# Optimization experiments

Measured on AMD Instinct MI355X. Metric: run time of the kernel, lower is better.

The kernel has to match this reference:

```python
import jax, jax.numpy as jnp
import numpy as np

H = 128
R = 14
B = 2048
TYPES = ['operator', 'table', 'column', 'predicate', 'operation', 'literal', 'numeral']
SIZES = {'operator': 100000, 'table': 20000, 'column': 120000, 'predicate': 60000,
         'operation': 100000, 'literal': 50000, 'numeral': 50000}
FEAT = {'operator': 4, 'table': 2, 'column': 10, 'predicate': 4, 'operation': 8,
        'literal': 1, 'numeral': 1}
# (name, src_type, dst_type, num_edges), order matches edge_type_mapping in the torch module
EDGES = [('ei_scannedby', 'table', 'operator', 100000),
         ('ei_pred_filters', 'predicate', 'operator', 100000),
         ('ei_outputby', 'column', 'operator', 100000),
         ('ei_col_connects', 'column', 'operation', 100000),
         ('ei_calledby', 'operator', 'operator', 100000),
         ('ei_op_filters', 'operation', 'operator', 100000),
         ('ei_op_connects', 'operation', 'predicate', 100000),
         ('ei_lit_connects', 'literal', 'operation', 100000),
         ('ei_num_connects', 'numeral', 'operation', 100000),
         ('ei_lit_self', 'literal', 'literal', 50000),
         ('ei_num_self', 'numeral', 'numeral', 50000),
         ('ei_tab_self', 'table', 'table', 20000),
         ('ei_col_self', 'column', 'column', 120000),
         ('ei_pred_self', 'predicate', 'predicate', 60000)]
OFFS = {}
_o = 0
for _t in TYPES:
    OFFS[_t] = _o
    _o += SIZES[_t]
N_TOTAL = _o


def setup_inputs():
    key = jax.random.key(0)
    ks = iter(jax.random.split(key, 64))
    inp = {}
    for t in TYPES:
        inp['x_' + t] = jax.random.normal(next(ks), (SIZES[t], FEAT[t]), jnp.float32)
    for name, s, d, E in EDGES:
        src = jax.random.randint(next(ks), (E,), 0, SIZES[s], jnp.int32)
        dst = jax.random.randint(next(ks), (E,), 0, SIZES[d], jnp.int32)
        inp[name] = jnp.stack([src, dst])
    inp['batch_operator'] = jnp.sort(
        jax.random.randint(next(ks), (SIZES['operator'],), 0, B, jnp.int32))

    def lin_w(k, din, dout):
        s = 1.0 / float(np.sqrt(din))
        return jax.random.uniform(k, (din, dout), jnp.float32, -s, s)

    for t in TYPES:
        inp['W_' + t] = lin_w(next(ks), FEAT[t], H)
        inp['b_' + t] = jnp.zeros((H,), jnp.float32)
    for c in ('c1', 'c2'):
        inp[c + '_root'] = lin_w(next(ks), H, H)
        inp[c + '_rel'] = jax.random.normal(next(ks), (R, H, H), jnp.float32) / float(np.sqrt(H))
        inp[c + '_bias'] = jnp.zeros((H,), jnp.float32)
    inp['n1_g'] = jnp.ones((H,), jnp.float32); inp['n1_b'] = jnp.zeros((H,), jnp.float32)
    inp['n2_g'] = jnp.ones((H,), jnp.float32); inp['n2_b'] = jnp.zeros((H,), jnp.float32)
    inp['W_lin'] = lin_w(next(ks), H, 1)
    inp['b_lin'] = jnp.zeros((1,), jnp.float32)
    return inp


def layer_norm(x, g, b, eps=1e-5):
    mu = jnp.mean(x, axis=-1, keepdims=True)
    var = jnp.var(x, axis=-1, keepdims=True)
    return (x - mu) * jax.lax.rsqrt(var + eps) * g + b


def rgcn(x, rel_edges, w_root, w_rel, bias):
    # PyG RGCNConv: root transform + per-relation gather -> GEMM -> scatter-mean into dst
    out = x @ w_root
    for r, (src, dst) in enumerate(rel_edges):
        msg = x[src] @ w_rel[r]  # [E_r, H]
        agg = jax.ops.segment_sum(msg, dst, num_segments=N_TOTAL)
        cnt = jax.ops.segment_sum(jnp.ones(src.shape, x.dtype), dst, num_segments=N_TOTAL)
        out = out + agg / jnp.maximum(cnt, 1.0)[:, None]
    return out + bias


def reference(x_operator, x_table, x_column, x_predicate, x_operation, x_literal, x_numeral,
              ei_scannedby, ei_pred_filters, ei_outputby, ei_col_connects, ei_calledby,
              ei_op_filters, ei_op_connects, ei_lit_connects, ei_num_connects, ei_lit_self,
              ei_num_self, ei_tab_self, ei_col_self, ei_pred_self, batch_operator,
              W_operator, b_operator, W_table, b_table, W_column, b_column,
              W_predicate, b_predicate, W_operation, b_operation, W_literal, b_literal,
              W_numeral, b_numeral, c1_root, c1_rel, c1_bias, c2_root, c2_rel, c2_bias,
              n1_g, n1_b, n2_g, n2_b, W_lin, b_lin):
    # per-node-type input embedding, then concat in fixed type order
    x = jnp.concatenate([
        x_operator @ W_operator + b_operator,
        x_table @ W_table + b_table,
        x_column @ W_column + b_column,
        x_predicate @ W_predicate + b_predicate,
        x_operation @ W_operation + b_operation,
        x_literal @ W_literal + b_literal,
        x_numeral @ W_numeral + b_numeral], axis=0)
    eis = [ei_scannedby, ei_pred_filters, ei_outputby, ei_col_connects, ei_calledby,
           ei_op_filters, ei_op_connects, ei_lit_connects, ei_num_connects, ei_lit_self,
           ei_num_self, ei_tab_self, ei_col_self, ei_pred_self]
    rel_edges = [(e[0] + OFFS[s], e[1] + OFFS[d]) for e, (_, s, d, _) in zip(eis, EDGES)]
    h = rgcn(x, rel_edges, c1_root, c1_rel, c1_bias)
    h = layer_norm(jax.nn.elu(h), n1_g, n1_b)  # dropout is identity in eval mode
    h = rgcn(h, rel_edges, c2_root, c2_rel, c2_bias)
    h = layer_norm(jax.nn.elu(h), n2_g, n2_b)
    op = h[:SIZES['operator']]  # operator offset is 0
    cnt = jax.ops.segment_sum(jnp.ones((op.shape[0],), op.dtype), batch_operator, num_segments=B)
    pooled = jax.ops.segment_sum(op, batch_operator, num_segments=B) / jnp.maximum(cnt, 1.0)[:, None]
    return (pooled @ W_lin + b_lin)[:, 0]  # [B]
```

## Files before the change

### kernel.cpp

```cpp
#include <hip/hip_runtime.h>
#include <hip/hip_bf16.h>
#include <math.h>

#define HD 128
#define N_OP 100000
#define N_L1 400000
#define NB 2048
#define CNT_TOT 1160000
#define EDG_TOT 1100000

typedef short short8 __attribute__((ext_vector_type(8)));
typedef float floatx4 __attribute__((ext_vector_type(4)));

static const int REL_E[14]    = {100000,100000,100000,100000,100000,100000,100000,100000,100000,50000,50000,20000,120000,60000};
static const int REL_DSZ[14]  = {100000,100000,100000,100000,100000,100000,60000,100000,100000,50000,50000,20000,120000,60000};
static const int CNT_OFF[14]  = {0,100000,200000,300000,400000,500000,600000,660000,760000,860000,910000,960000,980000,1100000};
static const int SRC_T[14] = {1,3,2,2,0,4,4,5,6,5,6,1,2,3};
static const int TF[7]  = {4,2,10,4,8,1,1};
static const size_t AGR_OFF[14] = {0,200000,600000,1600000,2600000,3000000,3800000,4280000,4380000,0,0,4480000,4520000,5720000};
#define AGR_TOT 5960000
static const int RELW[14] = {4,7,12,93,23,28,70,104,106,-1,-1,40,54,79};
static const int RELI[14] = {6,11,22,103,27,36,78,105,107,-1,-1,42,64,83};
static const int ROOTW[5] = {0,38,44,66,85};
static const int ROOTB[5] = {37,43,65,84,108};
#define WL1_ROWS 109

__device__ inline unsigned short f2bf(float f) {
  union { float f; unsigned int u; } v; v.f = f;
  unsigned int r = v.u + 0x7FFF + ((v.u >> 16) & 1);
  return (unsigned short)(r >> 16);
}
__device__ inline float bfu2f(unsigned short u) {
  union { unsigned int i; float f; } v; v.i = ((unsigned int)u) << 16; return v.f;
}

struct CJob { const int* dst; int coff; int E; int blk0; };
struct CPackK { CJob j[12]; int bblk0; const int* batch; float* pcnt; int nop; };

__global__ void count_k(CPackK P, int* __restrict__ ICNT) {
  int b = blockIdx.x;
  if (b >= P.bblk0) {
    int i = (b - P.bblk0) * 256 + threadIdx.x;
    if (i < P.nop) atomicAdd(&P.pcnt[P.batch[i]], 1.0f);
    return;
  }
  int ji = 0;
#pragma unroll
  for (int i = 1; i < 12; ++i) if (b >= P.j[i].blk0) ji = i;
  CJob J = P.j[ji];
  int e = (b - J.blk0) * 256 + threadIdx.x;
  if (e < J.E) atomicAdd(&ICNT[J.coff + J.dst[e]], 1);
}

#define SCAN_BLK 1024
__global__ void scan1(const int* __restrict__ in, int* __restrict__ out,
                      int* __restrict__ bsum, int n) {
  __shared__ int sh[256];
  int t = threadIdx.x;
  int base = blockIdx.x * SCAN_BLK + t * 4;
  int v0 = 0, v1 = 0, v2 = 0, v3 = 0;
  if (base + 3 < n) { int4 q = *(const int4*)&in[base]; v0 = q.x; v1 = q.y; v2 = q.z; v3 = q.w; }
  else {
    if (base < n) v0 = in[base];
    if (base + 1 < n) v1 = in[base + 1];
    if (base + 2 < n) v2 = in[base + 2];
    if (base + 3 < n) v3 = in[base + 3];
  }
  int ts = v0 + v1 + v2 + v3;
  sh[t] = ts; __syncthreads();
  for (int o = 1; o < 256; o <<= 1) {
    int x = (t >= o) ? sh[t - o] : 0;
    __syncthreads();
    sh[t] += x;
    __syncthreads();
  }
  int excl = sh[t] - ts;
  if (base < n) out[base] = excl;
  if (base + 1 < n) out[base + 1] = excl + v0;
  if (base + 2 < n) out[base + 2] = excl + v0 + v1;
  if (base + 3 < n) out[base + 3] = excl + v0 + v1 + v2;
  if (t == 255) bsum[blockIdx.x] = sh[255];
}

__global__ void scan2(int* __restrict__ bs, int nb) {
  __shared__ int sh[256];
  int t = threadIdx.x;
  const int C = 5;
  int v[C]; int ts = 0;
#pragma unroll
  for (int i = 0; i < C; ++i) { int idx = t * C + i; v[i] = (idx < nb) ? bs[idx] : 0; ts += v[i]; }
  sh[t] = ts; __syncthreads();
  for (int o = 1; o < 256; o <<= 1) {
    int x = (t >= o) ? sh[t - o] : 0;
    __syncthreads();
    sh[t] += x;
    __syncthreads();
  }
  int run = sh[t] - ts;
#pragma unroll
  for (int i = 0; i < C; ++i) { int idx = t * C + i; if (idx < nb) bs[idx] = run; run += v[i]; }
}

__global__ void scan3(int* __restrict__ CUR, int2* __restrict__ OFF2,
                      const int* __restrict__ ICNT, const int* __restrict__ bs, int n) {
  int i = blockIdx.x * 256 + threadIdx.x;
  if (i < n) {
    int o = CUR[i] + bs[i >> 10];
    CUR[i] = o;
    OFF2[i] = make_int2(o, ICNT[i]);
  }
}

struct FJob { const int* src; const int* dst; int coff; int E; int blk0; };
struct FPackK { FJob j[12]; };

__global__ void fill_k(FPackK P, int* __restrict__ CUR, int* __restrict__ EDG) {
  int b = blockIdx.x;
  int ji = 0;
#pragma unroll
  for (int i = 1; i < 12; ++i) if (b >= P.j[i].blk0) ji = i;
  FJob J = P.j[ji];
  int e = (b - J.blk0) * 256 + threadIdx.x;
  if (e < J.E) {
    int pos = atomicAdd(&CUR[J.coff + J.dst[e]], 1);
    EDG[pos] = J.src[e];
  }
}

struct GJob { const float* x; float* agr; int coff; int D; int F; int blk0; };
struct GPack { GJob j[12]; };

template <int F>
__device__ inline void gathF(const float* __restrict__ x, float* __restrict__ agr,
                             const int* __restrict__ EDG, int2 oc, int d) {
  if (oc.y == 0) return;
  float s[F];
#pragma unroll
  for (int f = 0; f < F; ++f) s[f] = 0.f;
  for (int e = 0; e < oc.y; ++e) {
    int si = EDG[oc.x + e];
    const float* xp = &x[(size_t)si * F];
#pragma unroll
    for (int f = 0; f < F; ++f) s[f] += xp[f];
  }
  float rc = 1.0f / (float)oc.y;
  float* ap = &agr[(size_t)d * F];
#pragma unroll
  for (int f = 0; f < F; ++f) ap[f] = s[f] * rc;
}

__global__ void gather_all(GPack P, const int2* __restrict__ OFF2, const int* __restrict__ EDG) {
  int b = blockIdx.x;
  int ji = 0;
#pragma unroll
  for (int i = 1; i < 12; ++i) if (b >= P.j[i].blk0) ji = i;
  GJob J = P.j[ji];
  int d = (b - J.blk0) * 256 + threadIdx.x;
  if (d >= J.D) return;
  int2 oc = OFF2[J.coff + d];
  switch (J.F) {
    case 1:  gathF<1>(J.x, J.agr, EDG, oc, d); break;
    case 2:  gathF<2>(J.x, J.agr, EDG, oc, d); break;
    case 4:  gathF<4>(J.x, J.agr, EDG, oc, d); break;
    case 8:  gathF<8>(J.x, J.agr, EDG, oc, d); break;
    default: gathF<10>(J.x, J.agr, EDG, oc, d); break;
  }
}

struct CombJob { const float* A; const float* bin; const float* Mtx; const float* extra; float* Wout; float* bout; int F; };
struct CombPack { CombJob j[17]; };

__global__ void weights_prep(CombPack P, const float* __restrict__ c2root,
                             const float* __restrict__ c2rel, __hip_bfloat16* __restrict__ Wt) {
  int b = blockIdx.x;
  if (b < 17) {
    if (threadIdx.x >= 128) return;
    CombJob J = P.j[b];
    int c = threadIdx.x;
    for (int f = 0; f <= J.F; ++f) {
      const float* arow = (f < J.F) ? &J.A[f * HD] : J.bin;
      float s = (f < J.F) ? 0.f : (J.extra ? J.extra[c] : 0.f);
      for (int k = 0; k < HD; ++k) s = fmaf(arow[k], J.Mtx[k * HD + c], s);
      if (f < J.F) J.Wout[f * HD + c] = s;
      else J.bout[c] = s;
    }
  } else {
    const int RID[6] = {-1, 0, 1, 2, 4, 5};
    int j = b - 17;
    const float* W = (j == 0) ? c2root : (c2rel + (size_t)RID[j] * HD * HD);
    __hip_bfloat16* o = Wt + (size_t)j * HD * 136;
    for (int i = threadIdx.x; i < HD * HD; i += 256) {
      int k = i >> 7, n = i & 127;
      o[n * 136 + k] = __float2bfloat16(W[i]);
    }
  }
}

struct L1v2 {
  const float* x0; const float* x1; const float* x2; const float* x3; const float* x4;
  const float* AGR; const float* WL1; const int2* OFF2;
  const float* g; const float* b;
  unsigned short* Hb;
};

__device__ inline void ldv2(float* s, const float* __restrict__ p) {
  float2 v = *(const float2*)p; s[0] = v.x; s[1] = v.y;
}
__device__ inline void ldv4(float* s, const float* __restrict__ p) {
  float4 v = *(const float4*)p; s[0] = v.x; s[1] = v.y; s[2] = v.z; s[3] = v.w;
}
__device__ inline void relF1(float* s, const float* __restrict__ agr,
                             const int2* __restrict__ OFF2, int cb, int row) {
  if (OFF2[cb + row].y > 0) { s[0] = agr[row]; s[1] = 1.f; }
  else { s[0] = 0.f; s[1] = 0.f; }
}
__device__ inline void relF2(float* s, const float* __restrict__ agr,
                             const int2* __restrict__ OFF2, int cb, int row) {
  if (OFF2[cb + row].y > 0) { ldv2(s, &agr[(size_t)row * 2]); s[2] = 1.f; }
  else { s[0] = s[1] = s[2] = 0.f; }
}
__device__ inline void relF4(float* s, const float* __restrict__ agr,
                             const int2* __restrict__ OFF2, int cb, int row) {
  if (OFF2[cb + row].y > 0) { ldv4(s, &agr[(size_t)row * 4]); s[4] = 1.f; }
  else {
#pragma unroll
    for (int f = 0; f < 5; ++f) s[f] = 0.f;
  }
}
__device__ inline void relF8(float* s, const float* __restrict__ agr,
                             const int2* __restrict__ OFF2, int cb, int row) {
  if (OFF2[cb + row].y > 0) {
    ldv4(s, &agr[(size_t)row * 8]); ldv4(s + 4, &agr[(size_t)row * 8 + 4]); s[8] = 1.f;
  } else {
#pragma unroll
    for (int f = 0; f < 9; ++f) s[f] = 0.f;
  }
}
__device__ inline void relF10(float* s, const float* __restrict__ agr,
                              const int2* __restrict__ OFF2, int cb, int row) {
  if (OFF2[cb + row].y > 0) {
    const float* p = &agr[(size_t)row * 10];
#pragma unroll
    for (int j = 0; j < 5; ++j) ldv2(s + 2 * j, p + 2 * j);
    s[10] = 1.f;
  } else {
#pragma unroll
    for (int f = 0; f < 11; ++f) s[f] = 0.f;
  }
}

template <int KT>
__device__ inline void l1_dot8(const float* __restrict__ Ls, const float (&s)[KT],
                               int c4, float (&a)[8]) {
  {
    float4 w0 = *(const float4*)&Ls[KT * 128 + c4];
    float4 w1 = *(const float4*)&Ls[KT * 128 + c4 + 64];
    a[0] = w0.x; a[1] = w0.y; a[2] = w0.z; a[3] = w0.w;
    a[4] = w1.x; a[5] = w1.y; a[6] = w1.z; a[7] = w1.w;
  }
#pragma unroll
  for (int k = 0; k < KT; ++k) {
    float4 w0 = *(const float4*)&Ls[k * 128 + c4];
    float4 w1 = *(const float4*)&Ls[k * 128 + c4 + 64];
    a[0] = fmaf(s[k], w0.x, a[0]); a[1] = fmaf(s[k], w0.y, a[1]);
    a[2] = fmaf(s[k], w0.z, a[2]); a[3] = fmaf(s[k], w0.w, a[3]);
    a[4] = fmaf(s[k], w1.x, a[4]); a[5] = fmaf(s[k], w1.y, a[5]);
    a[6] = fmaf(s[k], w1.z, a[6]); a[7] = fmaf(s[k], w1.w, a[7]);
  }
}

__device__ inline void l1_fin8(float (&a)[8], int c4, const float* __restrict__ g,
                               const float* __restrict__ bb,
                               unsigned short* __restrict__ Hb, int orow) {
  float p = 0.f, q = 0.f;
#pragma unroll
  for (int j = 0; j < 8; ++j) {
    a[j] = (a[j] > 0.f) ? a[j] : (expf(a[j]) - 1.f);
    p += a[j]; q += a[j] * a[j];
  }
#pragma unroll
  for (int m = 8; m >= 1; m >>= 1) {
    p += __shfl_xor(p, m, 64);
    q += __shfl_xor(q, m, 64);
  }
  float mean = p * (1.0f / HD);
  float var = q * (1.0f / HD) - mean * mean;
  float rstd = rsqrtf(var + 1e-5f);
  float4 g0 = *(const float4*)&g[c4], g1 = *(const float4*)&g[c4 + 64];
  float4 b0 = *(const float4*)&bb[c4], b1 = *(const float4*)&bb[c4 + 64];
  float gg[8] = {g0.x, g0.y, g0.z, g0.w, g1.x, g1.y, g1.z, g1.w};
  float bv[8] = {b0.x, b0.y, b0.z, b0.w, b1.x, b1.y, b1.z, b1.w};
  float o[8];
#pragma unroll
  for (int j = 0; j < 8; ++j) o[j] = (a[j] - mean) * rstd * gg[j] + bv[j];
  uint2 lo, hi;
  lo.x = (unsigned int)f2bf(o[0]) | ((unsigned int)f2bf(o[1]) << 16);
  lo.y = (unsigned int)f2bf(o[2]) | ((unsigned int)f2bf(o[3]) << 16);
  hi.x = (unsigned int)f2bf(o[4]) | ((unsigned int)f2bf(o[5]) << 16);
  hi.y = (unsigned int)f2bf(o[6]) | ((unsigned int)f2bf(o[7]) << 16);
  *(uint2*)&Hb[(size_t)orow * HD + c4] = lo;
  *(uint2*)&Hb[(size_t)orow * HD + c4 + 64] = hi;
}

__global__ __launch_bounds__(256) void layer1_v5(L1v2 A) {
  __shared__ float Ls[38 * 128];
  const int b = blockIdx.x, t = threadIdx.x;
  const int wv = t >> 6, ln = t & 63;
  const int sub = ln >> 4, c4 = (ln & 15) * 4;
  int type, seg;
  if (b < 1563) { type = 0; seg = b; }
  else if (b < 1876) { type = 1; seg = b - 1563; }
  else if (b < 3751) { type = 2; seg = b - 1876; }
  else if (b < 4689) { type = 3; seg = b - 3751; }
  else { type = 4; seg = b - 4689; }
  const int NR[5] = {38, 6, 22, 19, 24};
  const int RB[5] = {0, 38, 44, 66, 85};
  const int TR[5] = {100000, 20000, 120000, 60000, 100000};
  const int OB[5] = {0, 100000, 120000, 240000, 300000};
  {
    const float4* src = (const float4*)(A.WL1 + RB[type] * 128);
    float4* dst = (float4*)Ls;
    int n4 = NR[type] * 32;
    for (int i = t; i < n4; i += 256) dst[i] = src[i];
  }
  __syncthreads();
  const int row0 = seg * 64, M = TR[type], ob = OB[type];

  if (type == 0) {
#pragma unroll
    for (int it = 0; it < 4; ++it) {
      int row = row0 + it * 16 + wv * 4 + sub;
      if (row >= M) continue;
      float s[37];
      ldv4(s, &A.x0[(size_t)row * 4]);
      relF2(s + 4, A.AGR + 0, A.OFF2, 0, row);
      relF4(s + 7, A.AGR + 200000, A.OFF2, 100000, row);
      relF10(s + 12, A.AGR + 600000, A.OFF2, 200000, row);
      relF4(s + 23, A.AGR + 2600000, A.OFF2, 400000, row);
      relF8(s + 28, A.AGR + 3000000, A.OFF2, 500000, row);
      float a[8];
      l1_dot8<37>(Ls, s, c4, a);
      l1_fin8(a, c4, A.g, A.b, A.Hb, ob + row);
    }
  } else if (type == 1) {
#pragma unroll
    for (int it = 0; it < 4; ++it) {
      int row = row0 + it * 16 + wv * 4 + sub;
      if (row >= M) continue;
      float s[5];
      ldv2(s, &A.x1[(size_t)row * 2]);
      relF2(s + 2, A.AGR + 4480000, A.OFF2, 960000, row);
      float a[8];
      l1_dot8<5>(Ls, s, c4, a);
      l1_fin8(a, c4, A.g, A.b, A.Hb, ob + row);
    }
  } else if (type == 2) {
#pragma unroll
    for (int it = 0; it < 4; ++it) {
      int row = row0 + it * 16 + wv * 4 + sub;
      if (row >= M) continue;
      float s[21];
      const float* p = &A.x2[(size_t)row * 10];
#pragma unroll
      for (int j = 0; j < 5; ++j) ldv2(s + 2 * j, p + 2 * j);
      relF10(s + 10, A.AGR + 4520000, A.OFF2, 980000, row);
      float a[8];
      l1_dot8<21>(Ls, s, c4, a);
      l1_fin8(a, c4, A.g, A.b, A.Hb, ob + row);
    }
  } else if (type == 3) {
#pragma unroll
    for (int it = 0; it < 4; ++it) {
      int row = row0 + it * 16 + wv * 4 + sub;
      if (row >= M) continue;
      float s[18];
      ldv4(s, &A.x3[(size_t)row * 4]);
      relF8(s + 4, A.AGR + 3800000, A.OFF2, 600000, row);
      relF4(s + 13, A.AGR + 5720000, A.OFF2, 1100000, row);
      float a[8];
      l1_dot8<18>(Ls, s, c4, a);
      l1_fin8(a, c4, A.g, A.b, A.Hb, ob + row);
    }
  } else {
#pragma unroll
    for (int it = 0; it < 4; ++it) {
      int row = row0 + it * 16 + wv * 4 + sub;
      if (row >= M) continue;
      float s[23];
      ldv4(s, &A.x4[(size_t)row * 8]);
      ldv4(s + 4, &A.x4[(size_t)row * 8 + 4]);
      relF10(s + 8, A.AGR + 1600000, A.OFF2, 300000, row);
      relF1(s + 19, A.AGR + 4280000, A.OFF2, 660000, row);
      relF1(s + 21, A.AGR + 4380000, A.OFF2, 760000, row);
      float a[8];
      l1_dot8<23>(Ls, s, c4, a);
      l1_fin8(a, c4, A.g, A.b, A.Hb, ob + row);
    }
  }
}

__global__ __launch_bounds__(256, 3)
void l2_fused(const unsigned short* __restrict__ Hb, const unsigned short* __restrict__ Wall,
              const int2* __restrict__ OFF2, const int* __restrict__ EDG,
              const float* __restrict__ c2bias, const float* __restrict__ n2g,
              const float* __restrict__ n2b, const float* __restrict__ Wl,
              const int* __restrict__ batch, float* __restrict__ accb, int M) {
  const int CSR_OFF[5] = {0, 100000, 200000, 400000, 500000};
  const int SOFF[5]    = {100000, 240000, 120000, 0, 300000};
  __shared__ unsigned short Ws[128 * 136];
  const int t = threadIdx.x, wv = t >> 6, ln = t & 63;
  const int quad = ln >> 4, ln15 = ln & 15, q8 = quad * 8;
  const int m0 = blockIdx.x * 128;

  int2 ocs[2][5];
#pragma unroll
  for (int mt = 0; mt < 2; ++mt) {
    int rowA = m0 + (wv * 2 + mt) * 16 + ln15;
#pragma unroll
    for (int r = 0; r < 5; ++r)
      ocs[mt][r] = (rowA < M) ? OFF2[CSR_OFF[r] + rowA] : make_int2(0, 0);
  }

  float bias_c[8], gw[8];
  float pg = 0.f, pb = 0.f;
#pragma unroll
  for (int nt = 0; nt < 8; ++nt) {
    int col = nt * 16 + ln15;
    float wl = Wl[col], gc = n2g[col], bc = n2b[col];
    bias_c[nt] = c2bias[col];
    gw[nt] = gc * wl;
    pg += gc * wl;
    pb += bc * wl;
  }
#pragma unroll
  for (int m = 8; m >= 1; m >>= 1) {
    pg += __shfl_xor(pg, m, 64);
    pb += __shfl_xor(pb, m, 64);
  }

  floatx4 acc[2][8];
#pragma unroll
  for (int a = 0; a < 2; ++a)
#pragma unroll
    for (int b = 0; b < 8; ++b) acc[a][b] = (floatx4){0.f, 0.f, 0.f, 0.f};

  for (int term = 0; term < 6; ++term) {
    __syncthreads();
    {
      const uint4* wg = (const uint4*)(Wall + (size_t)term * 128 * 136);
      uint4* ws4 = (uint4*)Ws;
#pragma unroll
      for (int i = 0; i < 9; ++i) {
        int idx = i * 256 + t;
        if (idx < 2176) ws4[idx] = wg[idx];
      }
    }
    __syncthreads();

    short8 afr[2][4];
#pragma unroll
    for (int mt = 0; mt < 2; ++mt) {
      int rowA = m0 + (wv * 2 + mt) * 16 + ln15;
      if (term == 0) {
        if (rowA < M) {
#pragma unroll
          for (int k4 = 0; k4 < 4; ++k4)
            afr[mt][k4] = *(const short8*)&Hb[(size_t)rowA * HD + k4 * 32 + q8];
        } else {
#pragma unroll
          for (int k4 = 0; k4 < 4; ++k4)
#pragma unroll
            for (int j = 0; j < 8; ++j) afr[mt][k4][j] = 0;
        }
      } else {
        float sum[4][8];
#pragma unroll
        for (int k4 = 0; k4 < 4; ++k4)
#pragma unroll
          for (int j = 0; j < 8; ++j) sum[k4][j] = 0.f;
        int2 oc = ocs[mt][term - 1];
        if (oc.y > 0) {
          int so = SOFF[term - 1];
          for (int e = 0; e < oc.y; ++e) {
            size_t s = (size_t)(EDG[oc.x + e] + so);
#pragma unroll
            for (int k4 = 0; k4 < 4; ++k4) {
              short8 h = *(const short8*)&Hb[s * HD + k4 * 32 + q8];
#pragma unroll
              for (int j = 0; j < 8; ++j) sum[k4][j] += bfu2f((unsigned short)h[j]);
            }
          }
          float rc = 1.0f / (float)oc.y;
#pragma unroll
          for (int k4 = 0; k4 < 4; ++k4)
#pragma unroll
            for (int j = 0; j < 8; ++j) sum[k4][j] *= rc;
        }
#pragma unroll
        for (int k4 = 0; k4 < 4; ++k4)
#pragma unroll
          for (int j = 0; j < 8; ++j) afr[mt][k4][j] = (short)f2bf(sum[k4][j]);
      }
    }

#pragma unroll
    for (int nt = 0; nt < 8; ++nt) {
      int wrow = nt * 16 + ln15;
      short8 b0 = *(const short8*)&Ws[wrow * 136 + 0 + q8];
      short8 b1 = *(const short8*)&Ws[wrow * 136 + 32 + q8];
      short8 b2 = *(const short8*)&Ws[wrow * 136 + 64 + q8];
      short8 b3 = *(const short8*)&Ws[wrow * 136 + 96 + q8];
#pragma unroll
      for (int mt = 0; mt < 2; ++mt) {
        acc[mt][nt] = __builtin_amdgcn_mfma_f32_16x16x32_bf16(afr[mt][0], b0, acc[mt][nt], 0, 0, 0);
        acc[mt][nt] = __builtin_amdgcn_mfma_f32_16x16x32_bf16(afr[mt][1], b1, acc[mt][nt], 0, 0, 0);
        acc[mt][nt] = __builtin_amdgcn_mfma_f32_16x16x32_bf16(afr[mt][2], b2, acc[mt][nt], 0, 0, 0);
        acc[mt][nt] = __builtin_amdgcn_mfma_f32_16x16x32_bf16(afr[mt][3], b3, acc[mt][nt], 0, 0, 0);
      }
    }
  }

#pragma unroll
  for (int mt = 0; mt < 2; ++mt) {
#pragma unroll
    for (int r = 0; r < 4; ++r) {
      int rowD = m0 + (wv * 2 + mt) * 16 + quad * 4 + r;
      float p = 0.f, q = 0.f, s1 = 0.f;
#pragma unroll
      for (int nt = 0; nt < 8; ++nt) {
        float v = acc[mt][nt][r] + bias_c[nt];
        float e = (v > 0.f) ? v : (expf(v) - 1.f);
        p += e; q += e * e; s1 += e * gw[nt];
      }
#pragma unroll
      for (int m = 8; m >= 1; m >>= 1) {
        p += __shfl_xor(p, m, 64);
        q += __shfl_xor(q, m, 64);
        s1 += __shfl_xor(s1, m, 64);
      }
      if (ln15 == 0 && rowD < M) {
        float mean = p * (1.0f / HD);
        float var = q * (1.0f / HD) - mean * mean;
        float rstd = rsqrtf(var + 1e-5f);
        float o = rstd * (s1 - mean * pg) + pb;
        atomicAdd(&accb[batch[rowD]], o);
      }
    }
  }
}

__global__ void final_kernel(const float* __restrict__ accb, const float* __restrict__ pcnt,
                             const float* __restrict__ bl, float* __restrict__ out) {
  int b = blockIdx.x * 256 + threadIdx.x;
  if (b < NB) out[b] = accb[b] / fmaxf(pcnt[b], 1.0f) + bl[0];
}

extern "C" void kernel_launch(void* const* d_in, const int* in_sizes, int n_in,
                              void* d_out, int out_size, void* d_ws, size_t ws_size,
                              hipStream_t stream) {
  const float* xt[7];
  for (int t = 0; t < 7; ++t) xt[t] = (const float*)d_in[t];
  const int* ei[14];
  for (int r = 0; r < 14; ++r) ei[r] = (const int*)d_in[7 + r];
  const int* batch = (const int*)d_in[21];
  const float* Wemb[7]; const float* bemb[7];
  for (int t = 0; t < 7; ++t) { Wemb[t] = (const float*)d_in[22 + 2 * t]; bemb[t] = (const float*)d_in[23 + 2 * t]; }
  const float* c_root[2] = {(const float*)d_in[36], (const float*)d_in[39]};
  const float* c_rel[2]  = {(const float*)d_in[37], (const float*)d_in[40]};
  const float* c_bias[2] = {(const float*)d_in[38], (const float*)d_in[41]};
  const float* ng[2] = {(const float*)d_in[42], (const float*)d_in[44]};
  const float* nbv[2] = {(const float*)d_in[43], (const float*)d_in[45]};
  const float* Wlin = (const float*)d_in[46];
  const float* blin = (const float*)d_in[47];
  float* out = (float*)d_out;

  char* base = (char*)d_ws;
  size_t off = 0;
  auto alloc = [&](size_t bytes) -> void* {
    void* p = base + off;
    off += (bytes + 255) & ~(size_t)255;
    return p;
  };
  __hip_bfloat16* Hb = (__hip_bfloat16*)alloc((size_t)N_L1 * HD * 2);
  float* AGR  = (float*)alloc((size_t)AGR_TOT * 4);
  int*   ICNT = (int*)alloc((size_t)CNT_TOT * 4);
  int*   CUR  = (int*)alloc((size_t)CNT_TOT * 4);
  int2*  OFF2 = (int2*)alloc((size_t)CNT_TOT * 8);
  int*   EDG  = (int*)alloc((size_t)EDG_TOT * 4);
  int*   BS   = (int*)alloc((size_t)1152 * 4);
  float* WL1  = (float*)alloc((size_t)WL1_ROWS * 128 * 4);
  __hip_bfloat16* WT2 = (__hip_bfloat16*)alloc((size_t)6 * HD * 136 * 2);
  float* ACC  = (float*)alloc((size_t)NB * 4);
  float* PCNT = (float*)alloc((size_t)NB * 4);

  static const int l1_rels[12] = {0,1,2,3,4,5,6,7,8,11,12,13};

  hipMemsetAsync(ICNT, 0, (size_t)CNT_TOT * 4, stream);
  hipMemsetAsync(ACC, 0, (size_t)2 * NB * 4, stream);

  CPackK CP1;
  int blk = 0;
  for (int q = 0; q < 12; ++q) {
    int r = l1_rels[q];
    CP1.j[q].dst = ei[r] + REL_E[r];
    CP1.j[q].coff = CNT_OFF[r];
    CP1.j[q].E = REL_E[r];
    CP1.j[q].blk0 = blk;
    blk += (REL_E[r] + 255) / 256;
  }
  CP1.bblk0 = blk; CP1.batch = batch; CP1.pcnt = PCNT; CP1.nop = N_OP;
  blk += (N_OP + 255) / 256;
  count_k<<<blk, 256, 0, stream>>>(CP1, ICNT);

  int nb1 = (CNT_TOT + SCAN_BLK - 1) / SCAN_BLK;
  scan1<<<nb1, 256, 0, stream>>>(ICNT, CUR, BS, CNT_TOT);
  scan2<<<1, 256, 0, stream>>>(BS, nb1);
  scan3<<<(CNT_TOT + 255) / 256, 256, 0, stream>>>(CUR, OFF2, ICNT, BS, CNT_TOT);

  FPackK FP;
  blk = 0;
  for (int q = 0; q < 12; ++q) {
    int r = l1_rels[q];
    FP.j[q].src = ei[r];
    FP.j[q].dst = ei[r] + REL_E[r];
    FP.j[q].coff = CNT_OFF[r];
    FP.j[q].E = REL_E[r];
    FP.j[q].blk0 = blk;
    blk += (REL_E[r] + 255) / 256;
  }
  fill_k<<<blk, 256, 0, stream>>>(FP, CUR, EDG);

  CombPack CP;
  for (int q = 0; q < 12; ++q) {
    int r = l1_rels[q]; int t = SRC_T[r];
    CombJob& J = CP.j[q];
    J.A = Wemb[t]; J.bin = bemb[t]; J.Mtx = c_rel[0] + (size_t)r * HD * HD;
    J.extra = nullptr;
    J.Wout = WL1 + (size_t)RELW[r] * 128;
    J.bout = WL1 + (size_t)RELI[r] * 128;
    J.F = TF[t];
  }
  for (int t = 0; t < 5; ++t) {
    CombJob& J = CP.j[12 + t];
    J.A = Wemb[t]; J.bin = bemb[t]; J.Mtx = c_root[0];
    J.extra = c_bias[0];
    J.Wout = WL1 + (size_t)ROOTW[t] * 128;
    J.bout = WL1 + (size_t)ROOTB[t] * 128;
    J.F = TF[t];
  }
  weights_prep<<<23, 256, 0, stream>>>(CP, c_root[1], c_rel[1], WT2);

  GPack GP;
  blk = 0;
  for (int q = 0; q < 12; ++q) {
    int r = l1_rels[q]; int t = SRC_T[r];
    GP.j[q].x = xt[t];
    GP.j[q].agr = AGR + AGR_OFF[r];
    GP.j[q].coff = CNT_OFF[r];
    GP.j[q].D = REL_DSZ[r];
    GP.j[q].F = TF[t];
    GP.j[q].blk0 = blk;
    blk += (REL_DSZ[r] + 255) / 256;
  }
  gather_all<<<blk, 256, 0, stream>>>(GP, OFF2, EDG);

  L1v2 A;
  A.x0 = xt[0]; A.x1 = xt[1]; A.x2 = xt[2]; A.x3 = xt[3]; A.x4 = xt[4];
  A.AGR = AGR; A.WL1 = WL1; A.OFF2 = OFF2;
  A.g = ng[0]; A.b = nbv[0]; A.Hb = (unsigned short*)Hb;
  layer1_v5<<<6252, 256, 0, stream>>>(A);

  l2_fused<<<(N_OP + 127) / 128, 256, 0, stream>>>(
      (const unsigned short*)Hb, (const unsigned short*)WT2,
      OFF2, EDG, c_bias[1], ng[1], nbv[1], Wlin, batch, ACC, N_OP);

  final_kernel<<<(NB + 255) / 256, 256, 0, stream>>>(ACC, PCNT, blin, out);
}
```

Measured before the change: 652.5 us.

## Pre-swizzle layer-2 weights into MFMA fragment order and drop LDS staging

Weights for the second layer are now written by the prep kernel directly in per-lane MFMA B-fragment order, so each wave reads its B fragments straight from global memory (L2-cached) instead of staging them through shared memory with two barriers per term. Each wave now handles one 16-row tile instead of two, the block covers 64 rows, and launch bounds allow 4 blocks per CU. The aim is to remove the barrier stalls and shared-memory footprint so more waves can hide the latency of the irregular neighbour gathers. The cost is repeated global weight reads per wave and half the reuse of each B fragment across row tiles.

Result: faster. 602.7 us (-7.6%).

```diff
diff --git a/kernel.cpp b/kernel.cpp
--- a/kernel.cpp
+++ b/kernel.cpp
@@ -188,10 +188,16 @@
     const int RID[6] = {-1, 0, 1, 2, 4, 5};
     int j = b - 17;
     const float* W = (j == 0) ? c2root : (c2rel + (size_t)RID[j] * HD * HD);
-    __hip_bfloat16* o = Wt + (size_t)j * HD * 136;
-    for (int i = threadIdx.x; i < HD * HD; i += 256) {
-      int k = i >> 7, n = i & 127;
-      o[n * 136 + k] = __float2bfloat16(W[i]);
+    __hip_bfloat16* o = Wt + (size_t)j * 16384;
+    for (int i = threadIdx.x; i < 16384; i += 256) {
+      int i8 = i & 7;
+      int ln = (i >> 3) & 63;
+      int k4 = (i >> 9) & 3;
+      int nt = i >> 11;
+      int ln15 = ln & 15, quad = ln >> 4;
+      int k = k4 * 32 + quad * 8 + i8;
+      int n = nt * 16 + ln15;
+      o[i] = __float2bfloat16(W[k * 128 + n]);
     }
   }
 }
@@ -399,27 +405,23 @@
   }
 }
 
-__global__ __launch_bounds__(256, 3)
-void l2_fused(const unsigned short* __restrict__ Hb, const unsigned short* __restrict__ Wall,
+__global__ __launch_bounds__(256, 4)
+void l2_fused(const unsigned short* __restrict__ Hb, const unsigned short* __restrict__ Wt,
               const int2* __restrict__ OFF2, const int* __restrict__ EDG,
               const float* __restrict__ c2bias, const float* __restrict__ n2g,
               const float* __restrict__ n2b, const float* __restrict__ Wl,
               const int* __restrict__ batch, float* __restrict__ accb, int M) {
   const int CSR_OFF[5] = {0, 100000, 200000, 400000, 500000};
   const int SOFF[5]    = {100000, 240000, 120000, 0, 300000};
-  __shared__ unsigned short Ws[128 * 136];
   const int t = threadIdx.x, wv = t >> 6, ln = t & 63;
   const int quad = ln >> 4, ln15 = ln & 15, q8 = quad * 8;
-  const int m0 = blockIdx.x * 128;
-
-  int2 ocs[2][5];
-#pragma unroll
-  for (int mt = 0; mt < 2; ++mt) {
-    int rowA = m0 + (wv * 2 + mt) * 16 + ln15;
-#pragma unroll
-    for (int r = 0; r < 5; ++r)
-      ocs[mt][r] = (rowA < M) ? OFF2[CSR_OFF[r] + rowA] : make_int2(0, 0);
-  }
+  const int m0 = blockIdx.x * 64;
+  const int rowA = m0 + wv * 16 + ln15;
+
+  int2 ocs[5];
+#pragma unroll
+  for (int r = 0; r < 5; ++r)
+    ocs[r] = (rowA < M) ? OFF2[CSR_OFF[r] + rowA] : make_int2(0, 0);
 
   float bias_c[8], gw[8];
   float pg = 0.f, pb = 0.f;
@@ -438,113 +440,89 @@
     pb += __shfl_xor(pb, m, 64);
   }
 
-  floatx4 acc[2][8];
-#pragma unroll
-  for (int a = 0; a < 2; ++a)
-#pragma unroll
-    for (int b = 0; b < 8; ++b) acc[a][b] = (floatx4){0.f, 0.f, 0.f, 0.f};
+  floatx4 acc[8];
+#pragma unroll
+  for (int b = 0; b < 8; ++b) acc[b] = (floatx4){0.f, 0.f, 0.f, 0.f};
 
   for (int term = 0; term < 6; ++term) {
-    __syncthreads();
-    {
-      const uint4* wg = (const uint4*)(Wall + (size_t)term * 128 * 136);
-      uint4* ws4 = (uint4*)Ws;
-#pragma unroll
-      for (int i = 0; i < 9; ++i) {
-        int idx = i * 256 + t;
-        if (idx < 2176) ws4[idx] = wg[idx];
+    short8 afr[4];
+    if (term == 0) {
+      if (rowA < M) {
+#pragma unroll
+        for (int k4 = 0; k4 < 4; ++k4)
+          afr[k4] = *(const short8*)&Hb[(size_t)rowA * HD + k4 * 32 + q8];
+      } else {
+#pragma unroll
+        for (int k4 = 0; k4 < 4; ++k4)
+#pragma unroll
+          for (int j = 0; j < 8; ++j) afr[k4][j] = 0;
       }
-    }
-    __syncthreads();
-
-    short8 afr[2][4];
-#pragma unroll
-    for (int mt = 0; mt < 2; ++mt) {
-      int rowA = m0 + (wv * 2 + mt) * 16 + ln15;
-      if (term == 0) {
-        if (rowA < M) {
-#pragma unroll
-          for (int k4 = 0; k4 < 4; ++k4)
-            afr[mt][k4] = *(const short8*)&Hb[(size_t)rowA * HD + k4 * 32 + q8];
-        } else {
-#pragma unroll
-          for (int k4 = 0; k4 < 4; ++k4)
-#pragma unroll
-            for (int j = 0; j < 8; ++j) afr[mt][k4][j] = 0;
+    } else {
+      float sum[4][8];
+#pragma unroll
+      for (int k4 = 0; k4 < 4; ++k4)
+#pragma unroll
+        for (int j = 0; j < 8; ++j) sum[k4][j] = 0.f;
+      int2 oc = ocs[term - 1];
+      if (oc.y > 0) {
+        int so = SOFF[term - 1];
+        for (int e = 0; e < oc.y; ++e) {
+          size_t s = (size_t)(EDG[oc.x + e] + so);
+#pragma unroll
+          for (int k4 = 0; k4 < 4; ++k4) {
+            short8 h = *(const short8*)&Hb[s * HD + k4 * 32 + q8];
+#pragma unroll
+            for (int j = 0; j < 8; ++j) sum[k4][j] += bfu2f((unsigned short)h[j]);
+          }
         }
-      } else {
-        float sum[4][8];
+        float rc = 1.0f / (float)oc.y;
 #pragma unroll
         for (int k4 = 0; k4 < 4; ++k4)
 #pragma unroll
-          for (int j = 0; j < 8; ++j) sum[k4][j] = 0.f;
-        int2 oc = ocs[mt][term - 1];
-        if (oc.y > 0) {
-          int so = SOFF[term - 1];
-          for (int e = 0; e < oc.y; ++e) {
-            size_t s = (size_t)(EDG[oc.x + e] + so);
-#pragma unroll
-            for (int k4 = 0; k4 < 4; ++k4) {
-              short8 h = *(const short8*)&Hb[s * HD + k4 * 32 + q8];
-#pragma unroll
-              for (int j = 0; j < 8; ++j) sum[k4][j] += bfu2f((unsigned short)h[j]);
-            }
-          }
-          float rc = 1.0f / (float)oc.y;
-#pragma unroll
-          for (int k4 = 0; k4 < 4; ++k4)
-#pragma unroll
-            for (int j = 0; j < 8; ++j) sum[k4][j] *= rc;
-        }
-#pragma unroll
-        for (int k4 = 0; k4 < 4; ++k4)
-#pragma unroll
-          for (int j = 0; j < 8; ++j) afr[mt][k4][j] = (short)f2bf(sum[k4][j]);
+          for (int j = 0; j < 8; ++j) sum[k4][j] *= rc;
       }
-    }
-
+#pragma unroll
+      for (int k4 = 0; k4 < 4; ++k4)
+#pragma unroll
+        for (int j = 0; j < 8; ++j) afr[k4][j] = (short)f2bf(sum[k4][j]);
+    }
+
+    const unsigned short* wb = Wt + (size_t)term * 16384 + (size_t)ln * 8;
 #pragma unroll
     for (int nt = 0; nt < 8; ++nt) {
-      int wrow = nt * 16 + ln15;
-      short8 b0 = *(const short8*)&Ws[wrow * 136 + 0 + q8];
-      short8 b1 = *(const short8*)&Ws[wrow * 136 + 32 + q8];
-      short8 b2 = *(const short8*)&Ws[wrow * 136 + 64 + q8];
-      short8 b3 = *(const short8*)&Ws[wrow * 136 + 96 + q8];
-#pragma unroll
-      for (int mt = 0; mt < 2; ++mt) {
-        acc[mt][nt] = __builtin_amdgcn_mfma_f32_16x16x32_bf16(afr[mt][0], b0, acc[mt][nt], 0, 0, 0);
-        acc[mt][nt] = __builtin_amdgcn_mfma_f32_16x16x32_bf16(afr[mt][1], b1, acc[mt][nt], 0, 0, 0);
-        acc[mt][nt] = __builtin_amdgcn_mfma_f32_16x16x32_bf16(afr[mt][2], b2, acc[mt][nt], 0, 0, 0);
-        acc[mt][nt] = __builtin_amdgcn_mfma_f32_16x16x32_bf16(afr[mt][3], b3, acc[mt][nt], 0, 0, 0);
-      }
-    }
-  }
-
-#pragma unroll
-  for (int mt = 0; mt < 2; ++mt) {
-#pragma unroll
-    for (int r = 0; r < 4; ++r) {
-      int rowD = m0 + (wv * 2 + mt) * 16 + quad * 4 + r;
-      float p = 0.f, q = 0.f, s1 = 0.f;
-#pragma unroll
-      for (int nt = 0; nt < 8; ++nt) {
-        float v = acc[mt][nt][r] + bias_c[nt];
-        float e = (v > 0.f) ? v : (expf(v) - 1.f);
-        p += e; q += e * e; s1 += e * gw[nt];
-      }
-#pragma unroll
-      for (int m = 8; m >= 1; m >>= 1) {
-        p += __shfl_xor(p, m, 64);
-        q += __shfl_xor(q, m, 64);
-        s1 += __shfl_xor(s1, m, 64);
-      }
-      if (ln15 == 0 && rowD < M) {
-        float mean = p * (1.0f / HD);
-        float var = q * (1.0f / HD) - mean * mean;
-        float rstd = rsqrtf(var + 1e-5f);
-        float o = rstd * (s1 - mean * pg) + pb;
-        atomicAdd(&accb[batch[rowD]], o);
-      }
+      short8 b0 = *(const short8*)(wb + nt * 2048 + 0 * 512);
+      short8 b1 = *(const short8*)(wb + nt * 2048 + 1 * 512);
+      short8 b2 = *(const short8*)(wb + nt * 2048 + 2 * 512);
+      short8 b3 = *(const short8*)(wb + nt * 2048 + 3 * 512);
+      acc[nt] = __builtin_amdgcn_mfma_f32_16x16x32_bf16(afr[0], b0, acc[nt], 0, 0, 0);
+      acc[nt] = __builtin_amdgcn_mfma_f32_16x16x32_bf16(afr[1], b1, acc[nt], 0, 0, 0);
+      acc[nt] = __builtin_amdgcn_mfma_f32_16x16x32_bf16(afr[2], b2, acc[nt], 0, 0, 0);
+      acc[nt] = __builtin_amdgcn_mfma_f32_16x16x32_bf16(afr[3], b3, acc[nt], 0, 0, 0);
+    }
+  }
+
+#pragma unroll
+  for (int r = 0; r < 4; ++r) {
+    int rowD = m0 + wv * 16 + quad * 4 + r;
+    float p = 0.f, q = 0.f, s1 = 0.f;
+#pragma unroll
+    for (int nt = 0; nt < 8; ++nt) {
+      float v = acc[nt][r] + bias_c[nt];
+      float e = (v > 0.f) ? v : (expf(v) - 1.f);
+      p += e; q += e * e; s1 += e * gw[nt];
+    }
+#pragma unroll
+    for (int m = 8; m >= 1; m >>= 1) {
+      p += __shfl_xor(p, m, 64);
+      q += __shfl_xor(q, m, 64);
+      s1 += __shfl_xor(s1, m, 64);
+    }
+    if (ln15 == 0 && rowD < M) {
+      float mean = p * (1.0f / HD);
+      float var = q * (1.0f / HD) - mean * mean;
+      float rstd = rsqrtf(var + 1e-5f);
+      float o = rstd * (s1 - mean * pg) + pb;
+      atomicAdd(&accb[batch[rowD]], o);
     }
   }
 }
@@ -589,7 +567,7 @@
   int*   EDG  = (int*)alloc((size_t)EDG_TOT * 4);
   int*   BS   = (int*)alloc((size_t)1152 * 4);
   float* WL1  = (float*)alloc((size_t)WL1_ROWS * 128 * 4);
-  __hip_bfloat16* WT2 = (__hip_bfloat16*)alloc((size_t)6 * HD * 136 * 2);
+  __hip_bfloat16* WT3 = (__hip_bfloat16*)alloc((size_t)6 * 16384 * 2);
   float* ACC  = (float*)alloc((size_t)NB * 4);
   float* PCNT = (float*)alloc((size_t)NB * 4);
 
@@ -648,7 +626,7 @@
     J.bout = WL1 + (size_t)ROOTB[t] * 128;
     J.F = TF[t];
   }
-  weights_prep<<<23, 256, 0, stream>>>(CP, c_root[1], c_rel[1], WT2);
+  weights_prep<<<23, 256, 0, stream>>>(CP, c_root[1], c_rel[1], WT3);
 
   GPack GP;
   blk = 0;
@@ -670,8 +648,8 @@
   A.g = ng[0]; A.b = nbv[0]; A.Hb = (unsigned short*)Hb;
   layer1_v5<<<6252, 256, 0, stream>>>(A);
 
-  l2_fused<<<(N_OP + 127) / 128, 256, 0, stream>>>(
-      (const unsigned short*)Hb, (const unsigned short*)WT2,
+  l2_fused<<<(N_OP + 63) / 64, 256, 0, stream>>>(
+      (const unsigned short*)Hb, (const unsigned short*)WT3,
       OFF2, EDG, c_bias[1], ng[1], nbv[1], Wlin, batch, ACC, N_OP);
 
   final_kernel<<<(NB + 255) / 256, 256, 0, stream>>>(ACC, PCNT, blin, out);
```
